# Optimization experiments

Measured on AMD Instinct MI355X. Metric: run time of the kernel, lower is better.

The kernel has to match this reference:

```python
import jax, jax.numpy as jnp
import numpy as np

GROUPS = 32
EPS = 1e-6

def setup_inputs() -> dict:
    key = jax.random.key(0)
    ks = jax.random.split(key, 5)
    b, c, h, w = 2, 512, 64, 64
    x = jax.random.normal(ks[0], (b, c, h, w), dtype=jnp.float32)
    gn_gamma = jnp.ones((c,), dtype=jnp.float32)
    gn_beta = jnp.zeros((c,), dtype=jnp.float32)
    qkv_w = jax.random.normal(ks[1], (3 * c, c), dtype=jnp.float32) * (c ** -0.5)
    qkv_b = jax.random.normal(ks[2], (3 * c,), dtype=jnp.float32) * 0.01
    proj_w = jax.random.normal(ks[3], (c, c), dtype=jnp.float32) * (c ** -0.5)
    proj_b = jax.random.normal(ks[4], (c,), dtype=jnp.float32) * 0.01
    return {"x": x, "gn_gamma": gn_gamma, "gn_beta": gn_beta,
            "qkv_w": qkv_w, "qkv_b": qkv_b, "proj_w": proj_w, "proj_b": proj_b}

def group_norm(x, gamma, beta):
    b, c, h, w = x.shape
    xg = x.reshape(b, GROUPS, c // GROUPS, h, w)
    mean = xg.mean(axis=(2, 3, 4), keepdims=True)
    var = xg.var(axis=(2, 3, 4), keepdims=True)
    xg = (xg - mean) * jax.lax.rsqrt(var + EPS)
    x = xg.reshape(b, c, h, w)
    return x * gamma[None, :, None, None] + beta[None, :, None, None]

def reference(x, gn_gamma, gn_beta, qkv_w, qkv_b, proj_w, proj_b):
    b, c, h, w = x.shape
    hn = group_norm(x, gn_gamma, gn_beta)
    # 1x1 conv == per-pixel matmul over channels
    qkv = jnp.einsum('bchw,oc->bohw', hn, qkv_w) + qkv_b[None, :, None, None]
    q = qkv[:, :c].reshape(b, c, h * w)          # [b, c, n]
    k = qkv[:, c:2 * c].reshape(b, c, h * w)     # [b, c, n]
    v = qkv[:, 2 * c:].reshape(b, c, h * w)      # [b, c, n]
    scale = int(c) ** (-0.5)
    scores = jnp.einsum('bcn,bcm->bnm', q, k) * scale  # [b, n(query), m(key)]
    attn = jax.nn.softmax(scores, axis=2)
    out = jnp.einsum('bcm,bnm->bcn', v, attn).reshape(b, c, h, w)
    out = jnp.einsum('bchw,oc->bohw', out, proj_w) + proj_b[None, :, None, None]
    return x + out
```

## Files before the change

kernel.cpp:

```cpp
#include <hip/hip_runtime.h>

typedef __attribute__((ext_vector_type(8))) short bf16x8;
typedef __attribute__((ext_vector_type(4))) short bf16x4;
typedef __attribute__((ext_vector_type(4))) float f32x4;
typedef __attribute__((ext_vector_type(2))) float f32x2;

#define BATCH 2
#define CH    512
#define NPIX  4096
#define NSP   2
#define SPK   2048
#define KT    32

__device__ __forceinline__ unsigned short f2b(float f) {
    unsigned int u; __builtin_memcpy(&u, &f, 4);
    u = u + 0x7FFFu + ((u >> 16) & 1u);
    return (unsigned short)(u >> 16);
}
__device__ __forceinline__ float b2f(unsigned short h) {
    unsigned int u = ((unsigned int)h) << 16;
    float f; __builtin_memcpy(&f, &u, 4);
    return f;
}
__device__ __forceinline__ void gll16(void* lds, const void* g) {
    __builtin_amdgcn_global_load_lds(
        (const __attribute__((address_space(1))) void*)g,
        (__attribute__((address_space(3))) void*)lds, 16, 0, 0);
}

__global__ __launch_bounds__(256) void convert_kernel(
    const float* __restrict__ qkv_w, const float* __restrict__ proj_w,
    unsigned short* __restrict__ wbf)
{
    int i = blockIdx.x * 256 + threadIdx.x;
    float v; int row, c; unsigned short* ob;
    if (i < 786432) { v = qkv_w[i];          row = i >> 9;  c = i & 511; ob = wbf; }
    else            { int j = i - 786432; v = proj_w[j]; row = j >> 9; c = j & 511; ob = wbf + 786432; }
    size_t o = ((size_t)((((row >> 4) * 16 + (c >> 5)) * 4 + ((c >> 3) & 3)) * 16 + (row & 15))) * 8 + (c & 7);
    ob[o] = f2b(v);
}

__global__ __launch_bounds__(256) void stats1_kernel(
    const float* __restrict__ x, f32x2* __restrict__ part)
{
    int id = blockIdx.x;
    int bg = id >> 2, q = id & 3;
    int b = bg >> 5, g = bg & 31;
    const float* xp = x + ((size_t)b * CH + (size_t)g * 16 + q * 4) * NPIX;
    float s = 0.f, ss = 0.f;
    for (int i = threadIdx.x; i < 4 * NPIX; i += 256) {
        float v = xp[i]; s += v; ss += v * v;
    }
    for (int off = 32; off; off >>= 1) {
        s  += __shfl_down(s,  off, 64);
        ss += __shfl_down(ss, off, 64);
    }
    __shared__ float red[2][4];
    int wv = threadIdx.x >> 6;
    if ((threadIdx.x & 63) == 0) { red[0][wv] = s; red[1][wv] = ss; }
    __syncthreads();
    if (threadIdx.x == 0) {
        s  = red[0][0] + red[0][1] + red[0][2] + red[0][3];
        ss = red[1][0] + red[1][1] + red[1][2] + red[1][3];
        part[id] = (f32x2){s, ss};
    }
}

__global__ __launch_bounds__(64) void stats2_kernel(
    const f32x2* __restrict__ part, float* __restrict__ stats)
{
    int t = threadIdx.x;
    float s = 0.f, ss = 0.f;
    #pragma unroll
    for (int q = 0; q < 4; q++) { f32x2 p = part[t * 4 + q]; s += p[0]; ss += p[1]; }
    const float inv = 1.f / (16 * NPIX);
    float mean = s * inv;
    float var  = ss * inv - mean * mean;
    stats[t * 2 + 0] = mean;
    stats[t * 2 + 1] = rsqrtf(var + 1e-6f);
}

__global__ __launch_bounds__(256, 2) void qkv_kernel(
    const float* __restrict__ x,
    const unsigned short* __restrict__ wbf,
    const float* __restrict__ bias,
    const float* __restrict__ gamma,
    const float* __restrict__ beta,
    const float* __restrict__ stats,
    unsigned short* __restrict__ Q,
    unsigned short* __restrict__ K,
    unsigned short* __restrict__ V)
{
    __shared__ unsigned short hn[64][520];
    int b     = blockIdx.y;
    int third = blockIdx.z;
    int m0    = blockIdx.x * 64;
    int tid = threadIdx.x;
    {
        const float* xb = x + (size_t)b * CH * NPIX + m0;
        const float* st = stats + b * 64;
        int p4 = (tid & 15) * 4, cg = tid >> 4;
        for (int c0 = 0; c0 < CH; c0 += 16) {
            int c = c0 + cg;
            float mean = st[(c >> 4) * 2 + 0];
            float rstd = st[(c >> 4) * 2 + 1];
            float ga = gamma[c] * rstd;
            float be = beta[c] - mean * ga;
            f32x4 v = *(const f32x4*)(xb + (size_t)c * NPIX + p4);
            hn[p4 + 0][c] = f2b(v[0] * ga + be);
            hn[p4 + 1][c] = f2b(v[1] * ga + be);
            hn[p4 + 2][c] = f2b(v[2] * ga + be);
            hn[p4 + 3][c] = f2b(v[3] * ga + be);
        }
    }
    __syncthreads();

    int wv = tid >> 6, lane = tid & 63, ln = lane & 15, quad = lane >> 4;
    const float scale = 0.04419417382415922f;
    #pragma unroll
    for (int nt = 0; nt < 8; nt++) {
        int o = nt * 64 + wv * 16 + ln;
        int row = third * 512 + o;
        int rg  = third * 32 + nt * 4 + wv;
        const unsigned short* bp = wbf + (size_t)rg * 8192 + quad * 128 + ln * 8;
        bf16x8 wf[16];
        #pragma unroll
        for (int k = 0; k < 16; k++) wf[k] = *(const bf16x8*)(bp + k * 512);
        float bi = bias[row];
        #pragma unroll
        for (int qt = 0; qt < 4; qt++) {
            f32x4 acc = {0.f, 0.f, 0.f, 0.f};
            #pragma unroll
            for (int k = 0; k < 16; k++) {
                bf16x8 a = *(const bf16x8*)(&hn[qt * 16 + ln][quad * 8 + k * 32]);
                acc = __builtin_amdgcn_mfma_f32_16x16x32_bf16(a, wf[k], acc, 0, 0, 0);
            }
            int m = m0 + qt * 16 + quad * 4;
            if (third == 0) {
                #pragma unroll
                for (int r = 0; r < 4; r++)
                    Q[((size_t)b * NPIX + m + r) * CH + o] = f2b((acc[r] + bi) * scale);
            } else if (third == 1) {
                #pragma unroll
                for (int r = 0; r < 4; r++)
                    K[((size_t)b * NPIX + m + r) * CH + o] = f2b(acc[r] + bi);
            } else {
                bf16x4 pk;
                #pragma unroll
                for (int r = 0; r < 4; r++) pk[r] = f2b(acc[r] + bi);
                int grp = m & ~31;
                int s   = ((m & 15) >> 2) * 8 + ((m >> 4) & 1) * 4;
                *(bf16x4*)(V + ((size_t)b * CH + o) * NPIX + grp + s) = pk;
            }
        }
    }
}

__global__ __launch_bounds__(512, 2) void attn_kernel(
    const unsigned short* __restrict__ Qg,
    const unsigned short* __restrict__ Kg,
    const unsigned short* __restrict__ Vg,
    unsigned short* __restrict__ Opart,
    float* __restrict__ ml)
{
    __shared__ __align__(16) char sm[114688];
    char* const KB0 = sm;
    char* const KB1 = sm + 32768;
    char* const VB  = sm + 65536;
    char* const SX  = sm + 98304;

    int bid = blockIdx.x;
    int xcd = bid & 7;
    int b  = (xcd >> 1) & 1;
    int sp = xcd & 1;
    int q0 = (((bid >> 3) << 1) | (xcd >> 2)) << 6;
    int tid = threadIdx.x;
    int wv = tid >> 6, lane = tid & 63, ln = lane & 15, quad = lane >> 4;
    int qg = wv >> 1, cs = wv & 1;

    const unsigned short* K = Kg + ((size_t)b * NPIX + (size_t)sp * SPK) * CH;
    const unsigned short* V = Vg + (size_t)b * CH * NPIX + (size_t)sp * SPK;
    const unsigned short* Qp = Qg + ((size_t)(b * NPIX + q0 + qg * 16)) * CH;

    auto stageK = [&](char* buf, int kb) {
        #pragma unroll
        for (int j = 0; j < 4; j++) {
            int r = wv * 4 + j;
            gll16(buf + r * 1024,
                  K + (size_t)(kb + r) * CH + ((lane ^ (r & 7)) << 3));
        }
    };
    auto stageV = [&](int kb) {
        #pragma unroll
        for (int j = 0; j < 4; j++) {
            int r0 = wv * 64 + j * 16;
            int ch = r0 + (lane >> 2);
            gll16(VB + r0 * 64,
                  V + (size_t)ch * NPIX + kb + (((lane & 3) ^ ((ch >> 1) & 3)) << 3));
        }
    };

    stageK(KB0, 0);
    bf16x8 qf[8];
    #pragma unroll
    for (int kt = 0; kt < 8; kt++)
        qf[kt] = *(const bf16x8*)(Qp + (size_t)ln * CH + cs * 256 + kt * 32 + quad * 8);
    stageV(0);

    const int BK = ln * 1024 + ((quad ^ (ln & 3)) << 4) + (((ln >> 2) & 1) << 6) + cs * 512;
    const int BV = (cs * 256 + ln) * 64 + ((quad ^ ((ln >> 1) & 3)) << 4);
    const int sxo = ((quad ^ (ln & 3)) << 5) + (((ln >> 2) & 1) << 4);
    const int sxw = ((wv * 16 + ln) << 7) + sxo;
    const int sxr = (((wv ^ 1) * 16 + ln) << 7) + sxo;

    f32x4 O[16];
    #pragma unroll
    for (int i = 0; i < 16; i++) O[i] = (f32x4){0.f, 0.f, 0.f, 0.f};
    float m_reg = -1e30f, l_reg = 0.f;

    for (int it = 0; it < SPK / KT; ++it) {
        char* const KBc = (it & 1) ? KB1 : KB0;
        char* const KBn = (it & 1) ? KB0 : KB1;
        int nkb = ((it + 1) * KT) & (SPK - 1);

        stageK(KBn, nkb);

        asm volatile("s_waitcnt vmcnt(8)" ::: "memory");
        __builtin_amdgcn_s_barrier();

        const char* kE = KBc + BK;
        const char* kO = KBc + (BK ^ 64);
        f32x4 Sa = {0.f,0.f,0.f,0.f}, Sb = {0.f,0.f,0.f,0.f};
        __builtin_amdgcn_s_setprio(1);
        #pragma unroll
        for (int kt = 0; kt < 8; kt++) {
            const char* p = (kt & 1) ? kO : kE;
            bf16x8 k0 = *(const bf16x8*)(p + (kt >> 1) * 128);
            bf16x8 k1 = *(const bf16x8*)(p + (kt >> 1) * 128 + 16384);
            Sa = __builtin_amdgcn_mfma_f32_16x16x32_bf16(k0, qf[kt], Sa, 0, 0, 0);
            Sb = __builtin_amdgcn_mfma_f32_16x16x32_bf16(k1, qf[kt], Sb, 0, 0, 0);
        }
        __builtin_amdgcn_s_setprio(0);

        *(f32x4*)(SX + sxw)        = Sa;
        *(f32x4*)(SX + (sxw ^ 16)) = Sb;
        asm volatile("s_waitcnt vmcnt(4) lgkmcnt(0)" ::: "memory");
        __builtin_amdgcn_s_barrier();
        Sa += *(const f32x4*)(SX + sxr);
        Sb += *(const f32x4*)(SX + (sxr ^ 16));

        float mx = fmaxf(fmaxf(fmaxf(Sa[0],Sa[1]), fmaxf(Sa[2],Sa[3])),
                         fmaxf(fmaxf(Sb[0],Sb[1]), fmaxf(Sb[2],Sb[3])));
        mx = fmaxf(mx, __shfl_xor(mx, 16, 64));
        mx = fmaxf(mx, __shfl_xor(mx, 32, 64));
        if (!__all(mx <= m_reg + 8.f)) {
            float mnew  = fmaxf(m_reg, mx);
            float alpha = __expf(m_reg - mnew);
            l_reg *= alpha;
            #pragma unroll
            for (int ct = 0; ct < 16; ct++) {
                #pragma unroll
                for (int r = 0; r < 4; r++) O[ct][r] *= alpha;
            }
            m_reg = mnew;
        }
        float e0 = __expf(Sa[0]-m_reg), e1 = __expf(Sa[1]-m_reg);
        float e2 = __expf(Sa[2]-m_reg), e3 = __expf(Sa[3]-m_reg);
        float e4 = __expf(Sb[0]-m_reg), e5 = __expf(Sb[1]-m_reg);
        float e6 = __expf(Sb[2]-m_reg), e7 = __expf(Sb[3]-m_reg);
        float ts = ((e0+e1)+(e2+e3)) + ((e4+e5)+(e6+e7));
        ts += __shfl_xor(ts, 16, 64);
        ts += __shfl_xor(ts, 32, 64);
        l_reg += ts;
        bf16x8 pf;
        pf[0] = f2b(e0); pf[1] = f2b(e1); pf[2] = f2b(e2); pf[3] = f2b(e3);
        pf[4] = f2b(e4); pf[5] = f2b(e5); pf[6] = f2b(e6); pf[7] = f2b(e7);

        const char* vp = VB + BV;
        __builtin_amdgcn_s_setprio(1);
        #pragma unroll
        for (int ct = 0; ct < 16; ct++) {
            bf16x8 vv = *(const bf16x8*)(vp + ct * 1024);
            O[ct] = __builtin_amdgcn_mfma_f32_16x16x32_bf16(vv, pf, O[ct], 0, 0, 0);
        }
        __builtin_amdgcn_s_setprio(0);

        asm volatile("s_waitcnt lgkmcnt(0)" ::: "memory");
        __builtin_amdgcn_s_barrier();

        stageV(nkb);
    }
    asm volatile("s_waitcnt vmcnt(0)" ::: "memory");

    size_t n = (size_t)(b * NSP + sp) * NPIX + q0 + qg * 16 + ln;
    unsigned short* Ob = Opart + n * CH + cs * 256 + quad * 4;
    #pragma unroll
    for (int ct = 0; ct < 16; ct++) {
        bf16x4 pk;
        #pragma unroll
        for (int r = 0; r < 4; r++) pk[r] = f2b(O[ct][r]);
        *(bf16x4*)(Ob + ct * 16) = pk;
    }
    if (cs == 0 && quad == 0) {
        ml[n * 2 + 0] = m_reg;
        ml[n * 2 + 1] = l_reg;
    }
}

__global__ __launch_bounds__(512, 2) void merge_kernel(
    const float* __restrict__ x,
    const unsigned short* __restrict__ Opart,
    const float* __restrict__ ml,
    const unsigned short* __restrict__ pw,
    const float* __restrict__ pb,
    float* __restrict__ out)
{
    __shared__ __align__(16) unsigned short ao[32][520];
    int b  = blockIdx.y;
    int q0 = blockIdx.x * 32;
    int tid = threadIdx.x;
    int wv = tid >> 6, lane = tid & 63, ln = lane & 15, quad = lane >> 4;

    {
        int p = tid & 31, cs = tid >> 5;
        int n = q0 + p;
        size_t i0 = ((size_t)(b * NSP + 0) * NPIX + n) * 2;
        size_t i1 = ((size_t)(b * NSP + 1) * NPIX + n) * 2;
        float m0 = ml[i0], l0 = ml[i0 + 1];
        float m1 = ml[i1], l1 = ml[i1 + 1];
        float M  = fmaxf(m0, m1);
        float e0 = __expf(m0 - M), e1 = __expf(m1 - M);
        float den = l0 * e0 + l1 * e1;
        float w0 = e0 / den, w1 = e1 / den;
        const unsigned short* O0 = Opart + ((size_t)(b * NSP + 0) * NPIX + n) * CH;
        const unsigned short* O1 = Opart + ((size_t)(b * NSP + 1) * NPIX + n) * CH;
        #pragma unroll
        for (int k = 0; k < 4; k++) {
            int c = cs * 8 + k * 128;
            bf16x8 a0 = *(const bf16x8*)(O0 + c);
            bf16x8 a1 = *(const bf16x8*)(O1 + c);
            #pragma unroll
            for (int j = 0; j < 8; j++)
                ao[p][c + j] = f2b(b2f((unsigned short)a0[j]) * w0 +
                                   b2f((unsigned short)a1[j]) * w1);
        }
    }
    __syncthreads();

    #pragma unroll
    for (int nt = 0; nt < 4; nt++) {
        int o = wv * 64 + nt * 16 + ln;
        int rg = wv * 4 + nt;
        const unsigned short* bp = pw + (size_t)rg * 8192 + quad * 128 + ln * 8;
        bf16x8 wf[16];
        #pragma unroll
        for (int k = 0; k < 16; k++) wf[k] = *(const bf16x8*)(bp + k * 512);
        float bi = pb[o];
        #pragma unroll
        for (int qt = 0; qt < 2; qt++) {
            f32x4 acc = {0.f, 0.f, 0.f, 0.f};
            #pragma unroll
            for (int k = 0; k < 16; k++) {
                bf16x8 a = *(const bf16x8*)(&ao[qt * 16 + ln][quad * 8 + k * 32]);
                acc = __builtin_amdgcn_mfma_f32_16x16x32_bf16(a, wf[k], acc, 0, 0, 0);
            }
            size_t base = ((size_t)b * CH + o) * NPIX + q0 + qt * 16 + quad * 4;
            f32x4 xin = *(const f32x4*)(x + base);
            f32x4 o4;
            #pragma unroll
            for (int r = 0; r < 4; r++) o4[r] = xin[r] + acc[r] + bi;
            *(f32x4*)(out + base) = o4;
        }
    }
}

extern "C" void kernel_launch(void* const* d_in, const int* in_sizes, int n_in,
                              void* d_out, int out_size, void* d_ws, size_t ws_size,
                              hipStream_t stream)
{
    const float* x      = (const float*)d_in[0];
    const float* gn_g   = (const float*)d_in[1];
    const float* gn_b   = (const float*)d_in[2];
    const float* qkv_w  = (const float*)d_in[3];
    const float* qkv_b  = (const float*)d_in[4];
    const float* proj_w = (const float*)d_in[5];
    const float* proj_b = (const float*)d_in[6];
    float* out = (float*)d_out;

    unsigned short* ws  = (unsigned short*)d_ws;
    unsigned short* Kb  = ws;
    unsigned short* Vb  = ws + 4u * 1024 * 1024;
    unsigned short* Qb  = ws + 8u * 1024 * 1024;
    unsigned short* wbf = ws + 12u * 1024 * 1024;
    unsigned short* wp  = wbf + 786432;
    float* stats = (float*)(ws + 13u * 1024 * 1024);
    f32x2* part  = (f32x2*)(ws + 13u * 1024 * 1024 + 1024);
    float* ml    = (float*)(ws + 13u * 1024 * 1024 + 4096);
    unsigned short* Opart = ws + 13u * 1024 * 1024 + 4096 + 131072;

    convert_kernel<<<dim3(1048576 / 256), 256, 0, stream>>>(qkv_w, proj_w, wbf);
    stats1_kernel <<<dim3(256), 256, 0, stream>>>(x, part);
    stats2_kernel <<<dim3(1), 64, 0, stream>>>(part, stats);
    qkv_kernel    <<<dim3(NPIX / 64, BATCH, 3), 256, 0, stream>>>(
        x, wbf, qkv_b, gn_g, gn_b, stats, Qb, Kb, Vb);
    attn_kernel   <<<dim3(256), 512, 0, stream>>>(Qb, Kb, Vb, Opart, ml);
    merge_kernel  <<<dim3(NPIX / 32, BATCH), 512, 0, stream>>>(
        x, Opart, ml, wp, proj_b, out);
}
```

Measured before the change: 337.8 us.

## Fuse weight conversion with stats, fold stats finalize into QKV, vectorize Q/K stores

```diff
diff --git a/kernel.cpp b/kernel.cpp
--- a/kernel.cpp
+++ b/kernel.cpp
@@ -28,22 +28,21 @@
         (__attribute__((address_space(3))) void*)lds, 16, 0, 0);
 }
 
-__global__ __launch_bounds__(256) void convert_kernel(
+__global__ __launch_bounds__(256) void convstats_kernel(
     const float* __restrict__ qkv_w, const float* __restrict__ proj_w,
-    unsigned short* __restrict__ wbf)
+    const float* __restrict__ x,
+    unsigned short* __restrict__ wbf, f32x2* __restrict__ part)
 {
-    int i = blockIdx.x * 256 + threadIdx.x;
-    float v; int row, c; unsigned short* ob;
-    if (i < 786432) { v = qkv_w[i];          row = i >> 9;  c = i & 511; ob = wbf; }
-    else            { int j = i - 786432; v = proj_w[j]; row = j >> 9; c = j & 511; ob = wbf + 786432; }
-    size_t o = ((size_t)((((row >> 4) * 16 + (c >> 5)) * 4 + ((c >> 3) & 3)) * 16 + (row & 15))) * 8 + (c & 7);
-    ob[o] = f2b(v);
-}
-
-__global__ __launch_bounds__(256) void stats1_kernel(
-    const float* __restrict__ x, f32x2* __restrict__ part)
-{
-    int id = blockIdx.x;
+    if (blockIdx.x < 4096) {
+        int i = blockIdx.x * 256 + threadIdx.x;
+        float v; int row, c; unsigned short* ob;
+        if (i < 786432) { v = qkv_w[i];       row = i >> 9; c = i & 511; ob = wbf; }
+        else            { int j = i - 786432; v = proj_w[j]; row = j >> 9; c = j & 511; ob = wbf + 786432; }
+        size_t o = ((size_t)((((row >> 4) * 16 + (c >> 5)) * 4 + ((c >> 3) & 3)) * 16 + (row & 15))) * 8 + (c & 7);
+        ob[o] = f2b(v);
+        return;
+    }
+    int id = blockIdx.x - 4096;
     int bg = id >> 2, q = id & 3;
     int b = bg >> 5, g = bg & 31;
     const float* xp = x + ((size_t)b * CH + (size_t)g * 16 + q * 4) * NPIX;
@@ -66,44 +65,46 @@
     }
 }
 
-__global__ __launch_bounds__(64) void stats2_kernel(
-    const f32x2* __restrict__ part, float* __restrict__ stats)
-{
-    int t = threadIdx.x;
-    float s = 0.f, ss = 0.f;
-    #pragma unroll
-    for (int q = 0; q < 4; q++) { f32x2 p = part[t * 4 + q]; s += p[0]; ss += p[1]; }
-    const float inv = 1.f / (16 * NPIX);
-    float mean = s * inv;
-    float var  = ss * inv - mean * mean;
-    stats[t * 2 + 0] = mean;
-    stats[t * 2 + 1] = rsqrtf(var + 1e-6f);
-}
-
 __global__ __launch_bounds__(256, 2) void qkv_kernel(
     const float* __restrict__ x,
     const unsigned short* __restrict__ wbf,
     const float* __restrict__ bias,
     const float* __restrict__ gamma,
     const float* __restrict__ beta,
-    const float* __restrict__ stats,
+    const f32x2* __restrict__ part,
     unsigned short* __restrict__ Q,
     unsigned short* __restrict__ K,
     unsigned short* __restrict__ V)
 {
     __shared__ unsigned short hn[64][520];
+    __shared__ float st2[32][2];
     int b     = blockIdx.y;
     int third = blockIdx.z;
     int m0    = blockIdx.x * 64;
     int tid = threadIdx.x;
+
+    if (tid < 32) {
+        float s = 0.f, ss = 0.f;
+        #pragma unroll
+        for (int q = 0; q < 4; q++) {
+            f32x2 p = part[(b * 32 + tid) * 4 + q];
+            s += p[0]; ss += p[1];
+        }
+        const float inv = 1.f / (16 * NPIX);
+        float mean = s * inv;
+        float var  = ss * inv - mean * mean;
+        st2[tid][0] = mean;
+        st2[tid][1] = rsqrtf(var + 1e-6f);
+    }
+    __syncthreads();
+
     {
         const float* xb = x + (size_t)b * CH * NPIX + m0;
-        const float* st = stats + b * 64;
         int p4 = (tid & 15) * 4, cg = tid >> 4;
         for (int c0 = 0; c0 < CH; c0 += 16) {
             int c = c0 + cg;
-            float mean = st[(c >> 4) * 2 + 0];
-            float rstd = st[(c >> 4) * 2 + 1];
+            float mean = st2[c >> 4][0];
+            float rstd = st2[c >> 4][1];
             float ga = gamma[c] * rstd;
             float be = beta[c] - mean * ga;
             f32x4 v = *(const f32x4*)(xb + (size_t)c * NPIX + p4);
@@ -119,38 +120,52 @@
     const float scale = 0.04419417382415922f;
     #pragma unroll
     for (int nt = 0; nt < 8; nt++) {
-        int o = nt * 64 + wv * 16 + ln;
-        int row = third * 512 + o;
-        int rg  = third * 32 + nt * 4 + wv;
+        int obase = nt * 64 + wv * 16;
+        int rg    = third * 32 + nt * 4 + wv;
         const unsigned short* bp = wbf + (size_t)rg * 8192 + quad * 128 + ln * 8;
         bf16x8 wf[16];
         #pragma unroll
         for (int k = 0; k < 16; k++) wf[k] = *(const bf16x8*)(bp + k * 512);
-        float bi = bias[row];
-        #pragma unroll
-        for (int qt = 0; qt < 4; qt++) {
-            f32x4 acc = {0.f, 0.f, 0.f, 0.f};
-            #pragma unroll
-            for (int k = 0; k < 16; k++) {
-                bf16x8 a = *(const bf16x8*)(&hn[qt * 16 + ln][quad * 8 + k * 32]);
-                acc = __builtin_amdgcn_mfma_f32_16x16x32_bf16(a, wf[k], acc, 0, 0, 0);
-            }
-            int m = m0 + qt * 16 + quad * 4;
-            if (third == 0) {
+
+        if (third == 2) {
+            float bi = bias[1024 + obase + ln];
+            #pragma unroll
+            for (int qt = 0; qt < 4; qt++) {
+                f32x4 acc = {0.f, 0.f, 0.f, 0.f};
                 #pragma unroll
-                for (int r = 0; r < 4; r++)
-                    Q[((size_t)b * NPIX + m + r) * CH + o] = f2b((acc[r] + bi) * scale);
-            } else if (third == 1) {
-                #pragma unroll
-                for (int r = 0; r < 4; r++)
-                    K[((size_t)b * NPIX + m + r) * CH + o] = f2b(acc[r] + bi);
-            } else {
+                for (int k = 0; k < 16; k++) {
+                    bf16x8 a = *(const bf16x8*)(&hn[qt * 16 + ln][quad * 8 + k * 32]);
+                    acc = __builtin_amdgcn_mfma_f32_16x16x32_bf16(a, wf[k], acc, 0, 0, 0);
+                }
+                int m = m0 + qt * 16 + quad * 4;
                 bf16x4 pk;
                 #pragma unroll
                 for (int r = 0; r < 4; r++) pk[r] = f2b(acc[r] + bi);
                 int grp = m & ~31;
                 int s   = ((m & 15) >> 2) * 8 + ((m >> 4) & 1) * 4;
-                *(bf16x4*)(V + ((size_t)b * CH + o) * NPIX + grp + s) = pk;
+                *(bf16x4*)(V + ((size_t)b * CH + obase + ln) * NPIX + grp + s) = pk;
+            }
+        } else {
+            f32x4 bi4 = *(const f32x4*)(bias + third * 512 + obase + quad * 4);
+            unsigned short* dst = (third == 0) ? Q : K;
+            #pragma unroll
+            for (int qt = 0; qt < 4; qt++) {
+                f32x4 acc = {0.f, 0.f, 0.f, 0.f};
+                #pragma unroll
+                for (int k = 0; k < 16; k++) {
+                    bf16x8 a = *(const bf16x8*)(&hn[qt * 16 + ln][quad * 8 + k * 32]);
+                    acc = __builtin_amdgcn_mfma_f32_16x16x32_bf16(wf[k], a, acc, 0, 0, 0);
+                }
+                int n = m0 + qt * 16 + ln;
+                bf16x4 pk;
+                if (third == 0) {
+                    #pragma unroll
+                    for (int r = 0; r < 4; r++) pk[r] = f2b((acc[r] + bi4[r]) * scale);
+                } else {
+                    #pragma unroll
+                    for (int r = 0; r < 4; r++) pk[r] = f2b(acc[r] + bi4[r]);
+                }
+                *(bf16x4*)(dst + ((size_t)b * NPIX + n) * CH + obase + quad * 4) = pk;
             }
         }
     }
@@ -393,16 +408,13 @@
     unsigned short* Qb  = ws + 8u * 1024 * 1024;
     unsigned short* wbf = ws + 12u * 1024 * 1024;
     unsigned short* wp  = wbf + 786432;
-    float* stats = (float*)(ws + 13u * 1024 * 1024);
     f32x2* part  = (f32x2*)(ws + 13u * 1024 * 1024 + 1024);
     float* ml    = (float*)(ws + 13u * 1024 * 1024 + 4096);
     unsigned short* Opart = ws + 13u * 1024 * 1024 + 4096 + 131072;
 
-    convert_kernel<<<dim3(1048576 / 256), 256, 0, stream>>>(qkv_w, proj_w, wbf);
-    stats1_kernel <<<dim3(256), 256, 0, stream>>>(x, part);
-    stats2_kernel <<<dim3(1), 64, 0, stream>>>(part, stats);
+    convstats_kernel<<<dim3(4096 + 256), 256, 0, stream>>>(qkv_w, proj_w, x, wbf, part);
     qkv_kernel    <<<dim3(NPIX / 64, BATCH, 3), 256, 0, stream>>>(
-        x, wbf, qkv_b, gn_g, gn_b, stats, Qb, Kb, Vb);
+        x, wbf, qkv_b, gn_g, gn_b, part, Qb, Kb, Vb);
     attn_kernel   <<<dim3(256), 512, 0, stream>>>(Qb, Kb, Vb, Opart, ml);
     merge_kernel  <<<dim3(NPIX / 32, BATCH), 512, 0, stream>>>(
         x, Opart, ml, wp, proj_b, out);
```

Measured after the change: 271.4 us. 1.24x faster.
